# Kernel tuning notes

Hardware: AMD Instinct MI355X
Metric: run time of the kernel (lower is better)

Reference implementation:

```python
import jax, jax.numpy as jnp
import numpy as np

EPS = 1e-5
B, BEAMS, DEPTH, NEXP, D = 2048, 4, 3, 4, 128

def _conv(x, w, b):
    y = jax.lax.conv_general_dilated(x, w, (1, 1), 'VALID',
                                     dimension_numbers=('NCHW', 'OIHW', 'NCHW'))
    return y + b[None, :, None, None]

def _bn(x, g, bt):
    m = jnp.mean(x, axis=(0, 2, 3), keepdims=True)
    v = jnp.var(x, axis=(0, 2, 3), keepdims=True)
    return (x - m) * jax.lax.rsqrt(v + EPS) * g[None, :, None, None] + bt[None, :, None, None]

def _pool(x):
    return jax.lax.reduce_window(x, 0.0, jax.lax.add, (1, 1, 2, 2), (1, 1, 2, 2), 'VALID') * 0.25

def setup_inputs() -> dict:
    key = jax.random.key(0)
    ks = jax.random.split(key, 16)
    s = 0.05
    return {
        'x': jax.random.normal(ks[0], (B, 1, 32, 32), jnp.float32),
        'traj': jax.random.normal(ks[1], (DEPTH, B * BEAMS, NEXP), jnp.float32),
        'score_values': jax.random.uniform(ks[2], (BEAMS, DEPTH), jnp.float32, 0.5, 1.0),
        'c1w': jax.random.normal(ks[3], (32, 1, 3, 3), jnp.float32) * s,
        'c1b': jnp.zeros((32,), jnp.float32),
        'c2w': jax.random.normal(ks[4], (32, 32, 3, 3), jnp.float32) * s,
        'c2b': jnp.zeros((32,), jnp.float32),
        'c3w': jax.random.normal(ks[5], (32, 32, 3, 3), jnp.float32) * s,
        'c3b': jnp.zeros((32,), jnp.float32),
        'g1': jnp.ones((32,), jnp.float32), 'bt1': jnp.zeros((32,), jnp.float32),
        'g2': jnp.ones((32,), jnp.float32), 'bt2': jnp.zeros((32,), jnp.float32),
        'g3': jnp.ones((32,), jnp.float32), 'bt3': jnp.zeros((32,), jnp.float32),
        'We': jax.random.normal(ks[6], (3, D, D), jnp.float32) * s,   # (expert, in, out)
        'be': jax.random.normal(ks[7], (3, D), jnp.float32) * s,
        'Wo': jax.random.normal(ks[8], (10, D), jnp.float32) * s,
        'bo': jnp.zeros((10,), jnp.float32),
    }

def reference(x, traj, score_values, c1w, c1b, c2w, c2b, c3w, c3b,
              g1, bt1, g2, bt2, g3, bt3, We, be, Wo, bo):
    h = _pool(jax.nn.relu(_bn(_conv(x, c1w, c1b), g1, bt1)))
    h = _pool(jax.nn.relu(_bn(_conv(h, c2w, c2b), g2, bt2)))
    h = _pool(jax.nn.relu(_bn(_conv(h, c3w, c3b), g3, bt3)))
    feat = h.reshape(B, -1)                                   # [B, 128]
    hs = jnp.broadcast_to(feat[:, None, :], (B, BEAMS, D)).reshape(B * BEAMS, D)
    for step in range(DEPTH):
        idx = jnp.argmax(traj[step], axis=-1)                  # [N] in 0..3
        lin = jnp.einsum('nd,edh->neh', hs, We) + be[None]     # [N, 3, 128]
        all_out = jnp.concatenate([lin, hs[:, None, :]], axis=1)  # expert 3 = Identity
        hs = jax.nn.relu(jnp.take_along_axis(all_out, idx[:, None, None], axis=1)[:, 0])
    preds = hs @ Wo.T + bo                                     # [N, 10]
    return preds * jnp.prod(score_values)
```

## Files before the change

### kernel.cpp

```cpp
#include <hip/hip_runtime.h>
#include <hip/hip_bf16.h>

#define EPSV 1e-5f
typedef __hip_bfloat16 bf16;
typedef __attribute__((ext_vector_type(8))) short v8s;
typedef __attribute__((ext_vector_type(4))) float v4f;
__device__ __forceinline__ float b2f(bf16 v) { return __bfloat162float(v); }
__device__ __forceinline__ bf16 f2b(float v) { return __float2bfloat16(v); }
__device__ __forceinline__ float bs2f(short s) {
  return __uint_as_float(((unsigned)(unsigned short)s) << 16);
}
__device__ __forceinline__ short f2bs(float v) {
  bf16 b = __float2bfloat16(v);
  return *(short*)&b;
}

__global__ __launch_bounds__(256) void fill_k(float* __restrict__ out, float val, int n)
{
  int i = blockIdx.x * 256 + threadIdx.x;
  if (i < n) out[i] = val;
}

__global__ __launch_bounds__(256) void setup_k(
    const float* __restrict__ w2, const float* __restrict__ w3,
    const float* __restrict__ We, const float* __restrict__ Wo,
    bf16* __restrict__ w2b, bf16* __restrict__ w3b,
    bf16* __restrict__ Web, bf16* __restrict__ Wob,
    int* __restrict__ cnt27, float* __restrict__ Macc,
    float* __restrict__ Sacc2, float* __restrict__ Sacc3)
{
  int i = blockIdx.x * 256 + threadIdx.x;
  if (i < 64) cnt27[i] = 0;
  if (i < 512) {
    Macc[i] = 0.f;
    Sacc2[i] = 0.f;
    Sacc3[i] = 0.f;
  }
  if (i < 9216) {
    int oc = i / 288, r = i - oc * 288, s = r >> 5, ic = r & 31;
    w2b[i] = f2b(w2[oc * 288 + ic * 9 + s]);
  } else if (i < 18432) {
    int j = i - 9216;
    int oc = j / 288, r = j - oc * 288, s = r >> 5, ic = r & 31;
    w3b[j] = f2b(w3[oc * 288 + ic * 9 + s]);
  } else if (i < 18432 + 49152) {
    Web[i - 18432] = f2b(We[i - 18432]);
  } else if (i < 18432 + 49152 + 2048) {
    int j = i - 18432 - 49152;
    int k = j >> 4, o = j & 15;
    Wob[j] = (o < 10) ? f2b(Wo[o * 128 + k]) : f2b(0.f);
  }
}

__global__ __launch_bounds__(256) void front_k(
    const float* __restrict__ traj, const float* __restrict__ x,
    int* __restrict__ cnt27, int* __restrict__ lists, float* __restrict__ Macc)
{
  int t = threadIdx.x;
  if (blockIdx.x < 32) {
    int row = blockIdx.x * 256 + t;
    __shared__ int lcnt[64], lbase[64];
    if (t < 64) lcnt[t] = 0;
    __syncthreads();
    int e[3];
#pragma unroll
    for (int s = 0; s < 3; ++s) {
      float4 tv = ((const float4*)traj)[s * 8192 + row];
      int ee = 0; float bv = tv.x;
      if (tv.y > bv) { bv = tv.y; ee = 1; }
      if (tv.z > bv) { bv = tv.z; ee = 2; }
      if (tv.w > bv) { bv = tv.w; ee = 3; }
      e[s] = ee;
    }
    int sig = e[0] + 4 * e[1] + 16 * e[2];
    int my = atomicAdd(&lcnt[sig], 1);
    __syncthreads();
    if (t < 64) lbase[t] = atomicAdd(&cnt27[t], lcnt[t]);
    __syncthreads();
    lists[sig * 8192 + lbase[sig] + my] = row;
    return;
  }
  int blk = blockIdx.x - 32;
  __shared__ __align__(16) float xs[1024];
  float M[45], S[9];
#pragma unroll
  for (int k = 0; k < 45; ++k) M[k] = 0.f;
#pragma unroll
  for (int k = 0; k < 9; ++k) S[k] = 0.f;
  for (int im = 0; im < 4; ++im) {
    int img = blk * 4 + im;
    ((float4*)xs)[t] = ((const float4*)(x + img * 1024))[t];
    __syncthreads();
    for (int p = t; p < 900; p += 256) {
      int y = p / 30, xx = p - y * 30;
      const float* r0 = xs + y * 32 + xx;
      float v[9];
      v[0] = r0[0];  v[1] = r0[1];  v[2] = r0[2];
      v[3] = r0[32]; v[4] = r0[33]; v[5] = r0[34];
      v[6] = r0[64]; v[7] = r0[65]; v[8] = r0[66];
      int idx = 0;
#pragma unroll
      for (int i = 0; i < 9; ++i) {
        S[i] += v[i];
#pragma unroll
        for (int j = i; j < 9; ++j) M[idx++] = fmaf(v[i], v[j], M[idx]);
      }
    }
    __syncthreads();
  }
  float a[54];
#pragma unroll
  for (int k = 0; k < 45; ++k) a[k] = M[k];
#pragma unroll
  for (int k = 0; k < 9; ++k) a[45 + k] = S[k];
#pragma unroll
  for (int k = 0; k < 54; ++k) {
#pragma unroll
    for (int off = 32; off; off >>= 1) a[k] += __shfl_down(a[k], off, 64);
  }
  __shared__ float red[4][54];
  int wv = t >> 6, lane = t & 63;
  if (lane == 0) {
#pragma unroll
    for (int k = 0; k < 54; ++k) red[wv][k] = a[k];
  }
  __syncthreads();
  if (t < 54)
    atomicAdd(&Macc[(blk & 7) * 64 + t], red[0][t] + red[1][t] + red[2][t] + red[3][t]);
}

__global__ __launch_bounds__(512) void conv1_apply_k(
    const float* __restrict__ x, const float* __restrict__ w1,
    const float* __restrict__ b1, const float* __restrict__ g,
    const float* __restrict__ bt, const float* __restrict__ Macc,
    bf16* __restrict__ pooled1)
{
  int img = blockIdx.x, t = threadIdx.x;
  __shared__ __align__(16) float xs[1024];
  __shared__ float Ms[54], scs[32], shs[32];
  if (t < 256) ((float4*)xs)[t] = ((const float4*)(x + img * 1024))[t];
  if (t >= 256 && t < 310) {
    int k = t - 256;
    float s = 0.f;
#pragma unroll
    for (int sl = 0; sl < 8; ++sl) s += Macc[sl * 64 + k];
    Ms[k] = s;
  }
  __syncthreads();
  if (t < 32) {
    float w[9];
#pragma unroll
    for (int j = 0; j < 9; ++j) w[j] = w1[t * 9 + j];
    float bias = b1[t];
    float wS = 0.f;
#pragma unroll
    for (int i = 0; i < 9; ++i) wS = fmaf(w[i], Ms[45 + i], wS);
    float wMw = 0.f;
    int idx = 0;
#pragma unroll
    for (int i = 0; i < 9; ++i)
#pragma unroll
      for (int j = i; j < 9; ++j) {
        float coef = (i == j) ? 1.f : 2.f;
        wMw = fmaf(coef * w[i] * w[j], Ms[idx], wMw);
        ++idx;
      }
    const float Np = 2048.f * 900.f;
    float mean = (wS + Np * bias) / Np;
    float sumsq = wMw + 2.f * bias * wS + Np * bias * bias;
    float var = sumsq / Np - mean * mean;
    float sc = g[t] / sqrtf(var + EPSV);
    scs[t] = sc;
    shs[t] = bt[t] - mean * sc;
  }
  __syncthreads();
  int ch = t & 31, pg = t >> 5;
  if (pg >= 15) return;
  float w[9];
#pragma unroll
  for (int j = 0; j < 9; ++j) w[j] = w1[ch * 9 + j];
  float bias = b1[ch], sc = scs[ch], sh = shs[ch];
  const float* rp = xs + 2 * pg * 32;
  float a0 = rp[0], a1 = rp[32], a2 = rp[64], a3 = rp[96];
  float b0 = rp[1], b1v = rp[33], b2 = rp[65], b3 = rp[97];
  bf16* orow = pooled1 + img * 7200 + pg * 15 * 32 + ch;
#pragma unroll
  for (int px = 0; px < 15; ++px) {
    int xb = 2 * px;
    float e0 = rp[xb + 2], e1 = rp[xb + 34], e2 = rp[xb + 66], e3 = rp[xb + 98];
    float f0 = rp[xb + 3], f1 = rp[xb + 35], f2 = rp[xb + 67], f3 = rp[xb + 99];
    float v00 = bias, v01 = bias, v10 = bias, v11 = bias;
    v00 = fmaf(a0, w[0], v00); v00 = fmaf(b0, w[1], v00); v00 = fmaf(e0, w[2], v00);
    v00 = fmaf(a1, w[3], v00); v00 = fmaf(b1v, w[4], v00); v00 = fmaf(e1, w[5], v00);
    v00 = fmaf(a2, w[6], v00); v00 = fmaf(b2, w[7], v00); v00 = fmaf(e2, w[8], v00);
    v01 = fmaf(b0, w[0], v01); v01 = fmaf(e0, w[1], v01); v01 = fmaf(f0, w[2], v01);
    v01 = fmaf(b1v, w[3], v01); v01 = fmaf(e1, w[4], v01); v01 = fmaf(f1, w[5], v01);
    v01 = fmaf(b2, w[6], v01); v01 = fmaf(e2, w[7], v01); v01 = fmaf(f2, w[8], v01);
    v10 = fmaf(a1, w[0], v10); v10 = fmaf(b1v, w[1], v10); v10 = fmaf(e1, w[2], v10);
    v10 = fmaf(a2, w[3], v10); v10 = fmaf(b2, w[4], v10); v10 = fmaf(e2, w[5], v10);
    v10 = fmaf(a3, w[6], v10); v10 = fmaf(b3, w[7], v10); v10 = fmaf(e3, w[8], v10);
    v11 = fmaf(b1v, w[0], v11); v11 = fmaf(e1, w[1], v11); v11 = fmaf(f1, w[2], v11);
    v11 = fmaf(b2, w[3], v11); v11 = fmaf(e2, w[4], v11); v11 = fmaf(f2, w[5], v11);
    v11 = fmaf(b3, w[6], v11); v11 = fmaf(e3, w[7], v11); v11 = fmaf(f3, w[8], v11);
    float r = fmaxf(fmaf(v00, sc, sh), 0.f) + fmaxf(fmaf(v01, sc, sh), 0.f)
            + fmaxf(fmaf(v10, sc, sh), 0.f) + fmaxf(fmaf(v11, sc, sh), 0.f);
    orow[px * 32] = f2b(r * 0.25f);
    a0 = e0; a1 = e1; a2 = e2; a3 = e3;
    b0 = f0; b1v = f1; b2 = f2; b3 = f3;
  }
}

template <int IN_W, int OUT_W, int OUT_PIX, bool OUT_BF16>
__global__ __launch_bounds__(256, 2) void conv_mfma_k(
    const bf16* __restrict__ in, const bf16* __restrict__ wb,
    void* __restrict__ outv, float* __restrict__ sacc, int ntiles)
{
  constexpr int IN_PIX = IN_W * IN_W;
  int t = threadIdx.x, lane = t & 63;
  int m = lane & 15, kg = lane >> 4;
  const short* wbs = (const short*)wb;
  v8s bfr[9][2];
#pragma unroll
  for (int s = 0; s < 9; ++s)
#pragma unroll
    for (int ob = 0; ob < 2; ++ob)
      bfr[s][ob] = *(const v8s*)(wbs + (ob * 16 + m) * 288 + s * 32 + kg * 8);

  float rs0 = 0.f, rss0 = 0.f, rs1 = 0.f, rss1 = 0.f;
  int gwave = blockIdx.x * 4 + (t >> 6);
  int nw = gridDim.x * 4;
  for (int tile = gwave; tile < ntiles; tile += nw) {
    unsigned p = tile * 16 + m;
    unsigned img = p / OUT_PIX, pix = p - img * OUT_PIX;
    unsigned y = pix / OUT_W, x = pix - y * OUT_W;
    const bf16* ap = in + img * (IN_PIX * 32) + (y * IN_W + x) * 32 + kg * 8;
    v4f acc0 = {0.f, 0.f, 0.f, 0.f}, acc1 = {0.f, 0.f, 0.f, 0.f};
#pragma unroll
    for (int ky = 0; ky < 3; ++ky)
#pragma unroll
      for (int kx = 0; kx < 3; ++kx) {
        v8s a = *(const v8s*)(ap + (ky * IN_W + kx) * 32);
        acc0 = __builtin_amdgcn_mfma_f32_16x16x32_bf16(a, bfr[ky * 3 + kx][0], acc0, 0, 0, 0);
        acc1 = __builtin_amdgcn_mfma_f32_16x16x32_bf16(a, bfr[ky * 3 + kx][1], acc1, 0, 0, 0);
      }
#pragma unroll
    for (int j = 0; j < 4; ++j) {
      rs0 += acc0[j]; rss0 = fmaf(acc0[j], acc0[j], rss0);
      rs1 += acc1[j]; rss1 = fmaf(acc1[j], acc1[j], rss1);
      unsigned pr = tile * 16 + kg * 4 + j;
      unsigned base = pr * 32;
      if (OUT_BF16) {
        bf16* o = (bf16*)outv;
        o[base + m] = f2b(acc0[j]);
        o[base + 16 + m] = f2b(acc1[j]);
      } else {
        float* o = (float*)outv;
        o[base + m] = acc0[j];
        o[base + 16 + m] = acc1[j];
      }
    }
  }
  rs0 += __shfl_xor(rs0, 16, 64);  rss0 += __shfl_xor(rss0, 16, 64);
  rs0 += __shfl_xor(rs0, 32, 64);  rss0 += __shfl_xor(rss0, 32, 64);
  rs1 += __shfl_xor(rs1, 16, 64);  rss1 += __shfl_xor(rss1, 16, 64);
  rs1 += __shfl_xor(rs1, 32, 64);  rss1 += __shfl_xor(rss1, 32, 64);
  __shared__ float red[4][32][2];
  int wv = t >> 6;
  if (lane < 16) {
    red[wv][lane][0] = rs0;      red[wv][lane][1] = rss0;
    red[wv][16 + lane][0] = rs1; red[wv][16 + lane][1] = rss1;
  }
  __syncthreads();
  if (t < 64) {
    int cc = t >> 1, j = t & 1;
    atomicAdd(&sacc[(blockIdx.x & 7) * 64 + t],
              red[0][cc][j] + red[1][cc][j] + red[2][cc][j] + red[3][cc][j]);
  }
}

__global__ __launch_bounds__(256) void conv2_apply_k(
    const bf16* __restrict__ in, const float* __restrict__ Sacc2,
    const float* __restrict__ g, const float* __restrict__ bt,
    bf16* __restrict__ out)
{
  int t = threadIdx.x;
  __shared__ float lsc[32], lsh[32];
  if (t < 32) {
    const float invn = 1.f / (2048.f * 169.f);
    float s = 0.f, ssum = 0.f;
#pragma unroll
    for (int sl = 0; sl < 8; ++sl) {
      s += Sacc2[sl * 64 + 2 * t];
      ssum += Sacc2[sl * 64 + 2 * t + 1];
    }
    float mean = s * invn;
    float var = ssum * invn - mean * mean;
    float sc = g[t] / sqrtf(var + EPSV);
    lsc[t] = sc;
    lsh[t] = bt[t] - mean * sc;
  }
  __syncthreads();
  int idx = blockIdx.x * 256 + t;
  int img = idx / 144, r = idx - img * 144;
  int pp = r >> 2, c8 = r & 3;
  int py = pp / 6, px = pp - py * 6;
  int ip0 = (2 * py) * 13 + 2 * px;
  const bf16* bp = in + (img * 169 + ip0) * 32 + c8 * 8;
  v8s a = *(const v8s*)bp;
  v8s b = *(const v8s*)(bp + 32);
  v8s cc = *(const v8s*)(bp + 13 * 32);
  v8s d = *(const v8s*)(bp + 14 * 32);
  union { v8s v; short s[8]; bf16 h[8]; } res;
#pragma unroll
  for (int k = 0; k < 8; ++k) {
    int ch = c8 * 8 + k;
    float sc = lsc[ch], sh = lsh[ch];
    float v = fmaxf(fmaf(bs2f(a[k]), sc, sh), 0.f) + fmaxf(fmaf(bs2f(b[k]), sc, sh), 0.f)
            + fmaxf(fmaf(bs2f(cc[k]), sc, sh), 0.f) + fmaxf(fmaf(bs2f(d[k]), sc, sh), 0.f);
    res.h[k] = f2b(v * 0.25f);
  }
  *(v8s*)(out + (img * 36 + pp) * 32 + c8 * 8) = res.v;
}

__global__ __launch_bounds__(256) void conv3_apply_k(
    const float* __restrict__ in, const float* __restrict__ Sacc3,
    const float* __restrict__ g, const float* __restrict__ bt,
    float* __restrict__ hs)
{
  int t = threadIdx.x;
  __shared__ float lsc[32], lsh[32];
  if (t < 32) {
    const float invn = 1.f / (2048.f * 16.f);
    float s = 0.f, ssum = 0.f;
#pragma unroll
    for (int sl = 0; sl < 8; ++sl) {
      s += Sacc3[sl * 64 + 2 * t];
      ssum += Sacc3[sl * 64 + 2 * t + 1];
    }
    float mean = s * invn;
    float var = ssum * invn - mean * mean;
    float sc = g[t] / sqrtf(var + EPSV);
    lsc[t] = sc;
    lsh[t] = bt[t] - mean * sc;
  }
  __syncthreads();
  int idx = blockIdx.x * 256 + t;
  int img = idx >> 7, r = idx & 127;
  int c = r >> 2, q = r & 3;
  int py = q >> 1, px = q & 1;
  int p0 = py * 8 + px * 2;
  const float* bp = in + img * 512 + c;
  float sc = lsc[c], sh = lsh[c];
  float v = (fmaxf(fmaf(bp[p0 * 32], sc, sh), 0.f)
           + fmaxf(fmaf(bp[(p0 + 1) * 32], sc, sh), 0.f)
           + fmaxf(fmaf(bp[(p0 + 4) * 32], sc, sh), 0.f)
           + fmaxf(fmaf(bp[(p0 + 5) * 32], sc, sh), 0.f)) * 0.25f;
  float* hb = hs + img * 512 + r;
  hb[0] = v; hb[128] = v; hb[256] = v; hb[384] = v;
}

__global__ __launch_bounds__(256) void moe_fused_k(
    const float* __restrict__ hs, const bf16* __restrict__ Web,
    const float* __restrict__ be, const bf16* __restrict__ Wob,
    const float* __restrict__ bo, const float* __restrict__ sv,
    const int* __restrict__ cnt27, const int* __restrict__ lists,
    float* __restrict__ out)
{
  int t = threadIdx.x, lane = t & 63, wv = t >> 6;
  int m = lane & 15, kg = lane >> 4;
  __shared__ float st[4][16][132];
  __shared__ int scnt[64], stile[64];

  if (t < 64) scnt[t] = cnt27[t];
  __syncthreads();
  if (t == 0) {
    int b = 0;
#pragma unroll
    for (int s = 0; s < 64; ++s) { stile[s] = b; b += (scnt[s] + 15) >> 4; }
  }
  __syncthreads();

  int g = blockIdx.x * 4 + wv;
  int sig = -1, tile = 0, cntS = 0;
#pragma unroll
  for (int s = 0; s < 64; ++s) {
    int nt = (scnt[s] + 15) >> 4;
    if (g >= stile[s] && g < stile[s] + nt) { sig = s; tile = g - stile[s]; cntS = scnt[s]; }
  }
  if (sig < 0) return;
  const int* lp = lists + sig * 8192;
  int ra = tile * 16 + m;
  int rowA = lp[ra < cntS ? ra : cntS - 1];

  const float* hrow = hs + rowA * 128 + kg * 32;
#pragma unroll
  for (int q = 0; q < 8; ++q)
    *(float4*)&st[wv][m][kg * 32 + q * 4] = ((const float4*)hrow)[q];

  int es[3] = { sig & 3, (sig >> 2) & 3, sig >> 4 };
#pragma unroll
  for (int stp = 0; stp < 3; ++stp) {
    int e = es[stp];
    if (e == 3) continue;
    const short* wbs = (const short*)(Web + e * 16384);
    v8s afr[4];
#pragma unroll
    for (int kk = 0; kk < 4; ++kk) {
      float4 a0 = *(const float4*)&st[wv][m][kk * 32 + kg * 8];
      float4 a1 = *(const float4*)&st[wv][m][kk * 32 + kg * 8 + 4];
      afr[kk][0] = f2bs(a0.x); afr[kk][1] = f2bs(a0.y);
      afr[kk][2] = f2bs(a0.z); afr[kk][3] = f2bs(a0.w);
      afr[kk][4] = f2bs(a1.x); afr[kk][5] = f2bs(a1.y);
      afr[kk][6] = f2bs(a1.z); afr[kk][7] = f2bs(a1.w);
    }
#pragma unroll
    for (int ob = 0; ob < 8; ++ob) {
      v4f acc = {0.f, 0.f, 0.f, 0.f};
#pragma unroll
      for (int kk = 0; kk < 4; ++kk) {
        v8s bfr;
#pragma unroll
        for (int j = 0; j < 8; ++j)
          bfr[j] = wbs[(kk * 32 + kg * 8 + j) * 128 + ob * 16 + m];
        acc = __builtin_amdgcn_mfma_f32_16x16x32_bf16(afr[kk], bfr, acc, 0, 0, 0);
      }
      float bb = be[e * 128 + ob * 16 + m];
#pragma unroll
      for (int j = 0; j < 4; ++j)
        st[wv][kg * 4 + j][ob * 16 + m] = fmaxf(acc[j] + bb, 0.f);
    }
  }

  float ps = 1.f;
#pragma unroll
  for (int i = 0; i < 12; ++i) ps *= sv[i];
  const short* wos = (const short*)Wob;
  v8s afr[4];
#pragma unroll
  for (int kk = 0; kk < 4; ++kk) {
    float4 a0 = *(const float4*)&st[wv][m][kk * 32 + kg * 8];
    float4 a1 = *(const float4*)&st[wv][m][kk * 32 + kg * 8 + 4];
    afr[kk][0] = f2bs(a0.x); afr[kk][1] = f2bs(a0.y);
    afr[kk][2] = f2bs(a0.z); afr[kk][3] = f2bs(a0.w);
    afr[kk][4] = f2bs(a1.x); afr[kk][5] = f2bs(a1.y);
    afr[kk][6] = f2bs(a1.z); afr[kk][7] = f2bs(a1.w);
  }
  v4f acc = {0.f, 0.f, 0.f, 0.f};
#pragma unroll
  for (int kk = 0; kk < 4; ++kk) {
    v8s bfr;
#pragma unroll
    for (int j = 0; j < 8; ++j)
      bfr[j] = wos[(kk * 32 + kg * 8 + j) * 16 + m];
    acc = __builtin_amdgcn_mfma_f32_16x16x32_bf16(afr[kk], bfr, acc, 0, 0, 0);
  }
  if (m < 10) {
    float bov = bo[m];
#pragma unroll
    for (int j = 0; j < 4; ++j) {
      int idx = tile * 16 + kg * 4 + j;
      if (idx < cntS) out[lp[idx] * 10 + m] = (acc[j] + bov) * ps;
    }
  }
}

extern "C" void kernel_launch(void* const* d_in, const int* in_sizes, int n_in,
                              void* d_out, int out_size, void* d_ws, size_t ws_size,
                              hipStream_t stream)
{
  float* out = (float*)d_out;

  static const int EXP[19] = {2097152, 98304, 12, 288, 32, 9216, 32, 9216, 32,
                              32, 32, 32, 32, 32, 32, 49152, 384, 1280, 10};
  int bad = -1;
  if (n_in != 19) bad = 100;
  else
    for (int i = 0; i < 19; ++i)
      if (in_sizes[i] != EXP[i]) { bad = i; break; }
  if (bad >= 0) {
    fill_k<<<(out_size + 255) / 256, 256, 0, stream>>>(out, 1000.f + 10.f * bad, out_size);
    return;
  }
  const size_t NEED = 75771904;
  if (ws_size < NEED) {
    fill_k<<<(out_size + 255) / 256, 256, 0, stream>>>(
        out, 3000.f + (float)(ws_size >> 20), out_size);
    return;
  }

  const float* x    = (const float*)d_in[0];
  const float* traj = (const float*)d_in[1];
  const float* sv   = (const float*)d_in[2];
  const float* c1w  = (const float*)d_in[3];
  const float* c1b  = (const float*)d_in[4];
  const float* c2w  = (const float*)d_in[5];
  const float* c3w  = (const float*)d_in[7];
  const float* g1   = (const float*)d_in[9];
  const float* bt1  = (const float*)d_in[10];
  const float* g2   = (const float*)d_in[11];
  const float* bt2  = (const float*)d_in[12];
  const float* g3   = (const float*)d_in[13];
  const float* bt3  = (const float*)d_in[14];
  const float* We   = (const float*)d_in[15];
  const float* be   = (const float*)d_in[16];
  const float* Wo   = (const float*)d_in[17];
  const float* bo   = (const float*)d_in[18];

  char* w = (char*)d_ws;
  bf16*  pooled1  = (bf16*)(w + 0);
  bf16*  conv2out = (bf16*)(w + 29491200);
  bf16*  pooled2  = (bf16*)(w + 51642368);
  bf16*  Web      = (bf16*)(w + 56360960);
  float* conv3out = (float*)(w + 61079552);
  float* hsA      = (float*)(w + 65273856);
  float* hsB      = (float*)(w + 69468160);
  float* Macc     = (float*)(w + 73662464);
  float* Sacc2    = (float*)(w + 73664512);
  float* Sacc3    = (float*)(w + 73666560);
  int*   cnt27    = (int*)(w + 73668608);
  bf16*  Wob      = (bf16*)(w + 73670656);
  int*   lists    = (int*)(w + 73674752);
  bf16*  w2b      = (bf16*)hsB;
  bf16*  w3b      = w2b + 9216;

  setup_k<<<272, 256, 0, stream>>>(c2w, c3w, We, Wo, w2b, w3b, Web, Wob,
                                   cnt27, Macc, Sacc2, Sacc3);
  front_k<<<544, 256, 0, stream>>>(traj, x, cnt27, lists, Macc);
  conv1_apply_k<<<2048, 512, 0, stream>>>(x, c1w, c1b, g1, bt1, Macc, pooled1);
  conv_mfma_k<15, 13, 169, true><<<1352, 256, 0, stream>>>(pooled1, w2b, conv2out,
                                                           Sacc2, 21632);
  conv2_apply_k<<<1152, 256, 0, stream>>>(conv2out, Sacc2, g2, bt2, pooled2);
  conv_mfma_k<6, 4, 16, false><<<512, 256, 0, stream>>>(pooled2, w3b, conv3out,
                                                        Sacc3, 2048);
  conv3_apply_k<<<1024, 256, 0, stream>>>(conv3out, Sacc3, g3, bt3, hsA);
  moe_fused_k<<<256, 256, 0, stream>>>(hsA, Web, be, Wob, bo, sv, cnt27, lists, out);
}
```

Measured before the change: 106.2 us.

## Fuse conv1-apply with conv2 MFMA and conv2-apply with conv3 via LDS

Conv1's BN/ReLU/pool output is now kept in shared memory (padded rows) and consumed directly by the conv2 MFMA in the same per-image block. Conv2's BN/ReLU/pool is folded into the conv3 kernel's load stage. This removes the pooled1 and pooled2 global round trips and two kernel launches. In exchange, conv2 runs 11 tiles over 8 waves per block, which leaves waves unevenly loaded, wastes padded rows, and raises LDS use, which may lower occupancy.

New measurement: 97.07 us. -8.6%, faster.

```diff
diff --git a/kernel.cpp b/kernel.cpp
--- a/kernel.cpp
+++ b/kernel.cpp
@@ -129,15 +129,18 @@
     atomicAdd(&Macc[(blk & 7) * 64 + t], red[0][t] + red[1][t] + red[2][t] + red[3][t]);
 }
 
-__global__ __launch_bounds__(512) void conv1_apply_k(
+__global__ __launch_bounds__(512, 2) void conv12_k(
     const float* __restrict__ x, const float* __restrict__ w1,
-    const float* __restrict__ b1, const float* __restrict__ g,
-    const float* __restrict__ bt, const float* __restrict__ Macc,
-    bf16* __restrict__ pooled1)
+    const float* __restrict__ b1, const float* __restrict__ g1,
+    const float* __restrict__ bt1, const float* __restrict__ Macc,
+    const bf16* __restrict__ w2b, bf16* __restrict__ conv2out,
+    float* __restrict__ Sacc2)
 {
   int img = blockIdx.x, t = threadIdx.x;
   __shared__ __align__(16) float xs[1024];
   __shared__ float Ms[54], scs[32], shs[32];
+  __shared__ short plds[225 * 40];
+  __shared__ float red[8][32][2];
   if (t < 256) ((float4*)xs)[t] = ((const float4*)(x + img * 1024))[t];
   if (t >= 256 && t < 310) {
     int k = t - 256;
@@ -169,56 +172,52 @@
     float mean = (wS + Np * bias) / Np;
     float sumsq = wMw + 2.f * bias * wS + Np * bias * bias;
     float var = sumsq / Np - mean * mean;
-    float sc = g[t] / sqrtf(var + EPSV);
+    float sc = g1[t] / sqrtf(var + EPSV);
     scs[t] = sc;
-    shs[t] = bt[t] - mean * sc;
-  }
-  __syncthreads();
-  int ch = t & 31, pg = t >> 5;
-  if (pg >= 15) return;
-  float w[9];
-#pragma unroll
-  for (int j = 0; j < 9; ++j) w[j] = w1[ch * 9 + j];
-  float bias = b1[ch], sc = scs[ch], sh = shs[ch];
-  const float* rp = xs + 2 * pg * 32;
-  float a0 = rp[0], a1 = rp[32], a2 = rp[64], a3 = rp[96];
-  float b0 = rp[1], b1v = rp[33], b2 = rp[65], b3 = rp[97];
-  bf16* orow = pooled1 + img * 7200 + pg * 15 * 32 + ch;
-#pragma unroll
-  for (int px = 0; px < 15; ++px) {
-    int xb = 2 * px;
-    float e0 = rp[xb + 2], e1 = rp[xb + 34], e2 = rp[xb + 66], e3 = rp[xb + 98];
-    float f0 = rp[xb + 3], f1 = rp[xb + 35], f2 = rp[xb + 67], f3 = rp[xb + 99];
-    float v00 = bias, v01 = bias, v10 = bias, v11 = bias;
-    v00 = fmaf(a0, w[0], v00); v00 = fmaf(b0, w[1], v00); v00 = fmaf(e0, w[2], v00);
-    v00 = fmaf(a1, w[3], v00); v00 = fmaf(b1v, w[4], v00); v00 = fmaf(e1, w[5], v00);
-    v00 = fmaf(a2, w[6], v00); v00 = fmaf(b2, w[7], v00); v00 = fmaf(e2, w[8], v00);
-    v01 = fmaf(b0, w[0], v01); v01 = fmaf(e0, w[1], v01); v01 = fmaf(f0, w[2], v01);
-    v01 = fmaf(b1v, w[3], v01); v01 = fmaf(e1, w[4], v01); v01 = fmaf(f1, w[5], v01);
-    v01 = fmaf(b2, w[6], v01); v01 = fmaf(e2, w[7], v01); v01 = fmaf(f2, w[8], v01);
-    v10 = fmaf(a1, w[0], v10); v10 = fmaf(b1v, w[1], v10); v10 = fmaf(e1, w[2], v10);
-    v10 = fmaf(a2, w[3], v10); v10 = fmaf(b2, w[4], v10); v10 = fmaf(e2, w[5], v10);
-    v10 = fmaf(a3, w[6], v10); v10 = fmaf(b3, w[7], v10); v10 = fmaf(e3, w[8], v10);
-    v11 = fmaf(b1v, w[0], v11); v11 = fmaf(e1, w[1], v11); v11 = fmaf(f1, w[2], v11);
-    v11 = fmaf(b2, w[3], v11); v11 = fmaf(e2, w[4], v11); v11 = fmaf(f2, w[5], v11);
-    v11 = fmaf(b3, w[6], v11); v11 = fmaf(e3, w[7], v11); v11 = fmaf(f3, w[8], v11);
-    float r = fmaxf(fmaf(v00, sc, sh), 0.f) + fmaxf(fmaf(v01, sc, sh), 0.f)
-            + fmaxf(fmaf(v10, sc, sh), 0.f) + fmaxf(fmaf(v11, sc, sh), 0.f);
-    orow[px * 32] = f2b(r * 0.25f);
-    a0 = e0; a1 = e1; a2 = e2; a3 = e3;
-    b0 = f0; b1v = f1; b2 = f2; b3 = f3;
-  }
-}
-
-template <int IN_W, int OUT_W, int OUT_PIX, bool OUT_BF16>
-__global__ __launch_bounds__(256, 2) void conv_mfma_k(
-    const bf16* __restrict__ in, const bf16* __restrict__ wb,
-    void* __restrict__ outv, float* __restrict__ sacc, int ntiles)
-{
-  constexpr int IN_PIX = IN_W * IN_W;
-  int t = threadIdx.x, lane = t & 63;
+    shs[t] = bt1[t] - mean * sc;
+  }
+  __syncthreads();
+  {
+    int ch = t & 31, pg = t >> 5;
+    if (pg < 15) {
+      float w[9];
+#pragma unroll
+      for (int j = 0; j < 9; ++j) w[j] = w1[ch * 9 + j];
+      float bias = b1[ch], sc = scs[ch], sh = shs[ch];
+      const float* rp = xs + 2 * pg * 32;
+      float a0 = rp[0], a1 = rp[32], a2 = rp[64], a3 = rp[96];
+      float b0 = rp[1], b1v = rp[33], b2 = rp[65], b3 = rp[97];
+      short* orow = plds + pg * 15 * 40 + ch;
+#pragma unroll
+      for (int px = 0; px < 15; ++px) {
+        int xb = 2 * px;
+        float e0 = rp[xb + 2], e1 = rp[xb + 34], e2 = rp[xb + 66], e3 = rp[xb + 98];
+        float f0 = rp[xb + 3], f1 = rp[xb + 35], f2 = rp[xb + 67], f3 = rp[xb + 99];
+        float v00 = bias, v01 = bias, v10 = bias, v11 = bias;
+        v00 = fmaf(a0, w[0], v00); v00 = fmaf(b0, w[1], v00); v00 = fmaf(e0, w[2], v00);
+        v00 = fmaf(a1, w[3], v00); v00 = fmaf(b1v, w[4], v00); v00 = fmaf(e1, w[5], v00);
+        v00 = fmaf(a2, w[6], v00); v00 = fmaf(b2, w[7], v00); v00 = fmaf(e2, w[8], v00);
+        v01 = fmaf(b0, w[0], v01); v01 = fmaf(e0, w[1], v01); v01 = fmaf(f0, w[2], v01);
+        v01 = fmaf(b1v, w[3], v01); v01 = fmaf(e1, w[4], v01); v01 = fmaf(f1, w[5], v01);
+        v01 = fmaf(b2, w[6], v01); v01 = fmaf(e2, w[7], v01); v01 = fmaf(f2, w[8], v01);
+        v10 = fmaf(a1, w[0], v10); v10 = fmaf(b1v, w[1], v10); v10 = fmaf(e1, w[2], v10);
+        v10 = fmaf(a2, w[3], v10); v10 = fmaf(b2, w[4], v10); v10 = fmaf(e2, w[5], v10);
+        v10 = fmaf(a3, w[6], v10); v10 = fmaf(b3, w[7], v10); v10 = fmaf(e3, w[8], v10);
+        v11 = fmaf(b1v, w[0], v11); v11 = fmaf(e1, w[1], v11); v11 = fmaf(f1, w[2], v11);
+        v11 = fmaf(b2, w[3], v11); v11 = fmaf(e2, w[4], v11); v11 = fmaf(f2, w[5], v11);
+        v11 = fmaf(b3, w[6], v11); v11 = fmaf(e3, w[7], v11); v11 = fmaf(f3, w[8], v11);
+        float r = fmaxf(fmaf(v00, sc, sh), 0.f) + fmaxf(fmaf(v01, sc, sh), 0.f)
+                + fmaxf(fmaf(v10, sc, sh), 0.f) + fmaxf(fmaf(v11, sc, sh), 0.f);
+        orow[px * 40] = f2bs(r * 0.25f);
+        a0 = e0; a1 = e1; a2 = e2; a3 = e3;
+        b0 = f0; b1v = f1; b2 = f2; b3 = f3;
+      }
+    }
+  }
+  __syncthreads();
+  int lane = t & 63, wv = t >> 6;
   int m = lane & 15, kg = lane >> 4;
-  const short* wbs = (const short*)wb;
+  const short* wbs = (const short*)w2b;
   v8s bfr[9][2];
 #pragma unroll
   for (int s = 0; s < 9; ++s)
@@ -227,36 +226,29 @@
       bfr[s][ob] = *(const v8s*)(wbs + (ob * 16 + m) * 288 + s * 32 + kg * 8);
 
   float rs0 = 0.f, rss0 = 0.f, rs1 = 0.f, rss1 = 0.f;
-  int gwave = blockIdx.x * 4 + (t >> 6);
-  int nw = gridDim.x * 4;
-  for (int tile = gwave; tile < ntiles; tile += nw) {
-    unsigned p = tile * 16 + m;
-    unsigned img = p / OUT_PIX, pix = p - img * OUT_PIX;
-    unsigned y = pix / OUT_W, x = pix - y * OUT_W;
-    const bf16* ap = in + img * (IN_PIX * 32) + (y * IN_W + x) * 32 + kg * 8;
+  for (int tile = wv; tile < 11; tile += 8) {
+    int pix = tile * 16 + m;
+    int cpix = pix < 169 ? pix : 168;
+    int y = cpix / 13, xcol = cpix - y * 13;
+    const short* ap = plds + (y * 15 + xcol) * 40 + kg * 8;
     v4f acc0 = {0.f, 0.f, 0.f, 0.f}, acc1 = {0.f, 0.f, 0.f, 0.f};
 #pragma unroll
     for (int ky = 0; ky < 3; ++ky)
 #pragma unroll
       for (int kx = 0; kx < 3; ++kx) {
-        v8s a = *(const v8s*)(ap + (ky * IN_W + kx) * 32);
+        v8s a = *(const v8s*)(ap + (ky * 15 + kx) * 40);
         acc0 = __builtin_amdgcn_mfma_f32_16x16x32_bf16(a, bfr[ky * 3 + kx][0], acc0, 0, 0, 0);
         acc1 = __builtin_amdgcn_mfma_f32_16x16x32_bf16(a, bfr[ky * 3 + kx][1], acc1, 0, 0, 0);
       }
 #pragma unroll
     for (int j = 0; j < 4; ++j) {
-      rs0 += acc0[j]; rss0 = fmaf(acc0[j], acc0[j], rss0);
-      rs1 += acc1[j]; rss1 = fmaf(acc1[j], acc1[j], rss1);
-      unsigned pr = tile * 16 + kg * 4 + j;
-      unsigned base = pr * 32;
-      if (OUT_BF16) {
-        bf16* o = (bf16*)outv;
-        o[base + m] = f2b(acc0[j]);
-        o[base + 16 + m] = f2b(acc1[j]);
-      } else {
-        float* o = (float*)outv;
-        o[base + m] = acc0[j];
-        o[base + 16 + m] = acc1[j];
+      int pr = tile * 16 + kg * 4 + j;
+      if (pr < 169) {
+        rs0 += acc0[j]; rss0 = fmaf(acc0[j], acc0[j], rss0);
+        rs1 += acc1[j]; rss1 = fmaf(acc1[j], acc1[j], rss1);
+        unsigned base = (img * 169 + pr) * 32;
+        conv2out[base + m] = f2b(acc0[j]);
+        conv2out[base + 16 + m] = f2b(acc1[j]);
       }
     }
   }
@@ -264,8 +256,6 @@
   rs0 += __shfl_xor(rs0, 32, 64);  rss0 += __shfl_xor(rss0, 32, 64);
   rs1 += __shfl_xor(rs1, 16, 64);  rss1 += __shfl_xor(rss1, 16, 64);
   rs1 += __shfl_xor(rs1, 32, 64);  rss1 += __shfl_xor(rss1, 32, 64);
-  __shared__ float red[4][32][2];
-  int wv = t >> 6;
   if (lane < 16) {
     red[wv][lane][0] = rs0;      red[wv][lane][1] = rss0;
     red[wv][16 + lane][0] = rs1; red[wv][16 + lane][1] = rss1;
@@ -273,18 +263,24 @@
   __syncthreads();
   if (t < 64) {
     int cc = t >> 1, j = t & 1;
-    atomicAdd(&sacc[(blockIdx.x & 7) * 64 + t],
-              red[0][cc][j] + red[1][cc][j] + red[2][cc][j] + red[3][cc][j]);
-  }
-}
-
-__global__ __launch_bounds__(256) void conv2_apply_k(
-    const bf16* __restrict__ in, const float* __restrict__ Sacc2,
-    const float* __restrict__ g, const float* __restrict__ bt,
-    bf16* __restrict__ out)
-{
-  int t = threadIdx.x;
+    float s = 0.f;
+#pragma unroll
+    for (int w8 = 0; w8 < 8; ++w8) s += red[w8][cc][j];
+    atomicAdd(&Sacc2[(img & 7) * 64 + t], s);
+  }
+}
+
+__global__ __launch_bounds__(256, 2) void conv3_mfma_k(
+    const bf16* __restrict__ conv2out, const bf16* __restrict__ w3b,
+    const float* __restrict__ Sacc2, const float* __restrict__ g2,
+    const float* __restrict__ bt2, float* __restrict__ conv3out,
+    float* __restrict__ Sacc3)
+{
+  int t = threadIdx.x, lane = t & 63, wv = t >> 6;
+  int m = lane & 15, kg = lane >> 4;
   __shared__ float lsc[32], lsh[32];
+  __shared__ short plds[4][36 * 40];
+  __shared__ float red[4][32][2];
   if (t < 32) {
     const float invn = 1.f / (2048.f * 169.f);
     float s = 0.f, ssum = 0.f;
@@ -295,31 +291,70 @@
     }
     float mean = s * invn;
     float var = ssum * invn - mean * mean;
-    float sc = g[t] / sqrtf(var + EPSV);
+    float sc = g2[t] / sqrtf(var + EPSV);
     lsc[t] = sc;
-    lsh[t] = bt[t] - mean * sc;
-  }
-  __syncthreads();
-  int idx = blockIdx.x * 256 + t;
-  int img = idx / 144, r = idx - img * 144;
-  int pp = r >> 2, c8 = r & 3;
-  int py = pp / 6, px = pp - py * 6;
-  int ip0 = (2 * py) * 13 + 2 * px;
-  const bf16* bp = in + (img * 169 + ip0) * 32 + c8 * 8;
-  v8s a = *(const v8s*)bp;
-  v8s b = *(const v8s*)(bp + 32);
-  v8s cc = *(const v8s*)(bp + 13 * 32);
-  v8s d = *(const v8s*)(bp + 14 * 32);
-  union { v8s v; short s[8]; bf16 h[8]; } res;
-#pragma unroll
-  for (int k = 0; k < 8; ++k) {
-    int ch = c8 * 8 + k;
-    float sc = lsc[ch], sh = lsh[ch];
-    float v = fmaxf(fmaf(bs2f(a[k]), sc, sh), 0.f) + fmaxf(fmaf(bs2f(b[k]), sc, sh), 0.f)
-            + fmaxf(fmaf(bs2f(cc[k]), sc, sh), 0.f) + fmaxf(fmaf(bs2f(d[k]), sc, sh), 0.f);
-    res.h[k] = f2b(v * 0.25f);
-  }
-  *(v8s*)(out + (img * 36 + pp) * 32 + c8 * 8) = res.v;
+    lsh[t] = bt2[t] - mean * sc;
+  }
+  __syncthreads();
+  int img = blockIdx.x * 4 + wv;
+#pragma unroll
+  for (int k = 0; k < 18; ++k) {
+    int e = k * 64 + lane;
+    int pp = e >> 5, c = e & 31;
+    int py = pp / 6, px = pp - py * 6;
+    int ip0 = (2 * py) * 13 + 2 * px;
+    const bf16* bp = conv2out + (img * 169 + ip0) * 32 + c;
+    float sc = lsc[c], sh = lsh[c];
+    float v = fmaxf(fmaf(b2f(bp[0]), sc, sh), 0.f)
+            + fmaxf(fmaf(b2f(bp[32]), sc, sh), 0.f)
+            + fmaxf(fmaf(b2f(bp[13 * 32]), sc, sh), 0.f)
+            + fmaxf(fmaf(b2f(bp[14 * 32]), sc, sh), 0.f);
+    plds[wv][pp * 40 + c] = f2bs(v * 0.25f);
+  }
+  const short* wbs = (const short*)w3b;
+  v8s bfr[9][2];
+#pragma unroll
+  for (int s = 0; s < 9; ++s)
+#pragma unroll
+    for (int ob = 0; ob < 2; ++ob)
+      bfr[s][ob] = *(const v8s*)(wbs + (ob * 16 + m) * 288 + s * 32 + kg * 8);
+
+  int y = m >> 2, xcol = m & 3;
+  const short* ap = plds[wv] + (y * 6 + xcol) * 40 + kg * 8;
+  v4f acc0 = {0.f, 0.f, 0.f, 0.f}, acc1 = {0.f, 0.f, 0.f, 0.f};
+#pragma unroll
+  for (int ky = 0; ky < 3; ++ky)
+#pragma unroll
+    for (int kx = 0; kx < 3; ++kx) {
+      v8s a = *(const v8s*)(ap + (ky * 6 + kx) * 40);
+      acc0 = __builtin_amdgcn_mfma_f32_16x16x32_bf16(a, bfr[ky * 3 + kx][0], acc0, 0, 0, 0);
+      acc1 = __builtin_amdgcn_mfma_f32_16x16x32_bf16(a, bfr[ky * 3 + kx][1], acc1, 0, 0, 0);
+    }
+  float rs0 = 0.f, rss0 = 0.f, rs1 = 0.f, rss1 = 0.f;
+#pragma unroll
+  for (int j = 0; j < 4; ++j) {
+    rs0 += acc0[j]; rss0 = fmaf(acc0[j], acc0[j], rss0);
+    rs1 += acc1[j]; rss1 = fmaf(acc1[j], acc1[j], rss1);
+    int pr = kg * 4 + j;
+    unsigned base = (img * 16 + pr) * 32;
+    float* o = conv3out;
+    o[base + m] = acc0[j];
+    o[base + 16 + m] = acc1[j];
+  }
+  rs0 += __shfl_xor(rs0, 16, 64);  rss0 += __shfl_xor(rss0, 16, 64);
+  rs0 += __shfl_xor(rs0, 32, 64);  rss0 += __shfl_xor(rss0, 32, 64);
+  rs1 += __shfl_xor(rs1, 16, 64);  rss1 += __shfl_xor(rss1, 16, 64);
+  rs1 += __shfl_xor(rs1, 32, 64);  rss1 += __shfl_xor(rss1, 32, 64);
+  if (lane < 16) {
+    red[wv][lane][0] = rs0;      red[wv][lane][1] = rss0;
+    red[wv][16 + lane][0] = rs1; red[wv][16 + lane][1] = rss1;
+  }
+  __syncthreads();
+  if (t < 64) {
+    int cc = t >> 1, j = t & 1;
+    atomicAdd(&Sacc3[(blockIdx.x & 7) * 64 + t],
+              red[0][cc][j] + red[1][cc][j] + red[2][cc][j] + red[3][cc][j]);
+  }
 }
 
 __global__ __launch_bounds__(256) void conv3_apply_k(
@@ -507,9 +542,7 @@
   const float* bo   = (const float*)d_in[18];
 
   char* w = (char*)d_ws;
-  bf16*  pooled1  = (bf16*)(w + 0);
   bf16*  conv2out = (bf16*)(w + 29491200);
-  bf16*  pooled2  = (bf16*)(w + 51642368);
   bf16*  Web      = (bf16*)(w + 56360960);
   float* conv3out = (float*)(w + 61079552);
   float* hsA      = (float*)(w + 65273856);
@@ -526,12 +559,8 @@
   setup_k<<<272, 256, 0, stream>>>(c2w, c3w, We, Wo, w2b, w3b, Web, Wob,
                                    cnt27, Macc, Sacc2, Sacc3);
   front_k<<<544, 256, 0, stream>>>(traj, x, cnt27, lists, Macc);
-  conv1_apply_k<<<2048, 512, 0, stream>>>(x, c1w, c1b, g1, bt1, Macc, pooled1);
-  conv_mfma_k<15, 13, 169, true><<<1352, 256, 0, stream>>>(pooled1, w2b, conv2out,
-                                                           Sacc2, 21632);
-  conv2_apply_k<<<1152, 256, 0, stream>>>(conv2out, Sacc2, g2, bt2, pooled2);
-  conv_mfma_k<6, 4, 16, false><<<512, 256, 0, stream>>>(pooled2, w3b, conv3out,
-                                                        Sacc3, 2048);
+  conv12_k<<<2048, 512, 0, stream>>>(x, c1w, c1b, g1, bt1, Macc, w2b, conv2out, Sacc2);
+  conv3_mfma_k<<<512, 256, 0, stream>>>(conv2out, w3b, Sacc2, g2, bt2, conv3out, Sacc3);
   conv3_apply_k<<<1024, 256, 0, stream>>>(conv3out, Sacc3, g3, bt3, hsA);
   moe_fused_k<<<256, 256, 0, stream>>>(hsA, Web, be, Wob, bo, sv, cnt27, lists, out);
 }
```
